# Kernel optimization log

Hardware: AMD Instinct MI355X
Metric: run time of the kernel (lower is better)

## Reference

```python
import jax, jax.numpy as jnp
import numpy as np

B, S, D = 4, 2048, 1024
H = 16
DK = D // H  # 64

def setup_inputs() -> dict:
    key = jax.random.key(0)
    ks = jax.random.split(key, 5)
    scale = 0.02
    return {
        "x": jax.random.normal(ks[0], (B, S, D), dtype=jnp.float32),
        "Wq": jax.random.normal(ks[1], (D, D), dtype=jnp.float32) * scale,
        "Wk": jax.random.normal(ks[2], (D, D), dtype=jnp.float32) * scale,
        "Wv": jax.random.normal(ks[3], (D, D), dtype=jnp.float32) * scale,
        "Wo": jax.random.normal(ks[4], (D, D), dtype=jnp.float32) * scale,
    }

def reference(x, Wq, Wk, Wv, Wo):
    b, s, d = x.shape
    h, dk = H, DK
    # torch nn.Linear(bias=False): y = x @ W.T
    q = (x @ Wq.T).reshape(b, s, h, dk).transpose(0, 2, 1, 3)  # [b,h,s,dk]
    k = (x @ Wk.T).reshape(b, s, h, dk).transpose(0, 2, 1, 3)
    v = (x @ Wv.T).reshape(b, s, h, dk).transpose(0, 2, 1, 3)
    scores = jnp.einsum('bhqd,bhkd->bhqk', q, k) * (dk ** -0.5)
    causal = jnp.triu(jnp.ones((s, s), dtype=bool), k=1)  # True = masked out
    scores = jnp.where(causal, -jnp.inf, scores)
    probs = jax.nn.softmax(scores, axis=-1)
    attn = jnp.einsum('bhqk,bhkd->bhqd', probs, v)  # [b,h,s,dk]
    attn = attn.transpose(0, 2, 1, 3).reshape(b, s, d)
    return attn @ Wo.T
```

## Files before the change

kernel.cpp:

```cpp
#include <hip/hip_runtime.h>

typedef __attribute__((ext_vector_type(8))) short bf16x8;
typedef __attribute__((ext_vector_type(4))) float f32x4;
typedef unsigned int u32;
typedef unsigned short u16;

constexpr int Bb = 4, S = 2048, D = 1024, H = 16, DK = 64, M = Bb * S;

__device__ __forceinline__ u16 f2bf(float f) {
  u32 u = __float_as_uint(f);
  return (u16)((u + 0x7fffu + ((u >> 16) & 1u)) >> 16);
}

__device__ __forceinline__ void gld_lds16(const u16* g, u16* l) {
  __builtin_amdgcn_global_load_lds((const __attribute__((address_space(1))) u32*)g,
                                   (__attribute__((address_space(3))) u32*)l, 16, 0, 0);
}

__global__ void cast_kernel(const float* __restrict__ s, u16* __restrict__ d, int n) {
  int i = (blockIdx.x * blockDim.x + threadIdx.x) * 4;
  if (i >= n) return;
  float4 f = *(const float4*)(s + i);
  ushort4 o;
  o.x = f2bf(f.x); o.y = f2bf(f.y); o.z = f2bf(f.z); o.w = f2bf(f.w);
  *(ushort4*)(d + i) = o;
}

struct CastArgs { const float* s[4]; u16* d[4]; };
__global__ void cast4_kernel(CastArgs a) {
  int i = (blockIdx.x * blockDim.x + threadIdx.x) * 4;
  int w = i >> 20;
  int off = i & ((1 << 20) - 1);
  float4 f = *(const float4*)(a.s[w] + off);
  ushort4 o;
  o.x = f2bf(f.x); o.y = f2bf(f.y); o.z = f2bf(f.z); o.w = f2bf(f.w);
  *(ushort4*)(a.d[w] + off) = o;
}

template <bool OUTF32>
__device__ __forceinline__ void gemm_core(const u16* __restrict__ A,
                                          const u16* __restrict__ Bt,
                                          float* __restrict__ Cf, u16* __restrict__ Cb,
                                          int Nn, int Kk, int m0, int n0,
                                          u16* As, u16* Bs) {
  const int tid = threadIdx.x, wave = tid >> 6, lane = tid & 63;
  const int quad = lane >> 4, col = lane & 15;
  const int wm = wave >> 1, wn = wave & 1;

  f32x4 acc[4][4];
#pragma unroll
  for (int i = 0; i < 4; i++)
#pragma unroll
    for (int j = 0; j < 4; j++) acc[i][j] = (f32x4){0.f, 0.f, 0.f, 0.f};

  for (int k0 = 0; k0 < Kk; k0 += 32) {
#pragma unroll
    for (int j = 0; j < 2; j++) {
      int cb = j * 256 + wave * 64;
      int c = cb + lane;
      const u16* ga = A + (size_t)(m0 + (c >> 2)) * Kk + k0 + (c & 3) * 8;
      gld_lds16(ga, &As[cb * 8]);
      const u16* gb = Bt + (size_t)(n0 + (c >> 2)) * Kk + k0 + (c & 3) * 8;
      gld_lds16(gb, &Bs[cb * 8]);
    }
    __syncthreads();
    bf16x8 af[4], bfr[4];
#pragma unroll
    for (int mi = 0; mi < 4; mi++)
      af[mi] = *(const bf16x8*)&As[(wm * 64 + mi * 16 + col) * 32 + quad * 8];
#pragma unroll
    for (int ni = 0; ni < 4; ni++)
      bfr[ni] = *(const bf16x8*)&Bs[(wn * 64 + ni * 16 + col) * 32 + quad * 8];
#pragma unroll
    for (int mi = 0; mi < 4; mi++)
#pragma unroll
      for (int ni = 0; ni < 4; ni++)
        acc[mi][ni] = __builtin_amdgcn_mfma_f32_16x16x32_bf16(af[mi], bfr[ni], acc[mi][ni], 0, 0, 0);
    __syncthreads();
  }
#pragma unroll
  for (int mi = 0; mi < 4; mi++)
#pragma unroll
    for (int ni = 0; ni < 4; ni++)
#pragma unroll
      for (int r = 0; r < 4; r++) {
        int row = m0 + wm * 64 + mi * 16 + quad * 4 + r;
        int cc = n0 + wn * 64 + ni * 16 + col;
        float v = acc[mi][ni][r];
        if (OUTF32) Cf[(size_t)row * Nn + cc] = v;
        else Cb[(size_t)row * Nn + cc] = f2bf(v);
      }
}

struct QkvArgs { const u16* bt[3]; u16* c[3]; };
__global__ __launch_bounds__(256) void gemm_qkv(const u16* __restrict__ A, QkvArgs q) {
  __shared__ __align__(16) u16 As[128 * 32];
  __shared__ __align__(16) u16 Bs[128 * 32];
  int sel = blockIdx.x >> 3;
  int n0 = (blockIdx.x & 7) * 128, m0 = blockIdx.y * 128;
  gemm_core<false>(A, q.bt[sel], nullptr, q.c[sel], D, D, m0, n0, As, Bs);
}

__global__ __launch_bounds__(256) void gemm_f32(const u16* __restrict__ A,
                                                const u16* __restrict__ Bt,
                                                float* __restrict__ C) {
  __shared__ __align__(16) u16 As[128 * 32];
  __shared__ __align__(16) u16 Bs[128 * 32];
  gemm_core<true>(A, Bt, C, nullptr, D, D, blockIdx.y * 128, blockIdx.x * 128, As, Bs);
}

__global__ __launch_bounds__(256) void attn_kernel(const u16* __restrict__ Q,
                                                   const u16* __restrict__ K,
                                                   const u16* __restrict__ V,
                                                   u16* __restrict__ O) {
  __shared__ __align__(16) u16 Ks[2][2][64 * 32];
  __shared__ __align__(16) u16 Vt[2][64 * 64];
  __shared__ __align__(16) u16 Pw[4][32 * 64];
  const int tid = threadIdx.x, wave = tid >> 6, lane = tid & 63;
  const int quad = lane >> 4, col = lane & 15;
  const int bh = blockIdx.x, b = bh >> 4, h = bh & 15;
  const int qb = (S / 128 - 1) - blockIdx.y;
  const size_t base = (size_t)b * S * D + h * DK;
  const int qw = qb * 128 + wave * 32;

  bf16x8 aq[2][2];
#pragma unroll
  for (int mi = 0; mi < 2; mi++)
#pragma unroll
    for (int kb = 0; kb < 2; kb++)
      aq[mi][kb] = *(const bf16x8*)(Q + base + (size_t)(qw + mi * 16 + col) * D + kb * 32 + quad * 8);

  f32x4 ao[2][4];
#pragma unroll
  for (int mi = 0; mi < 2; mi++)
#pragma unroll
    for (int dg = 0; dg < 4; dg++) ao[mi][dg] = (f32x4){0.f, 0.f, 0.f, 0.f};
  float lp[2][4];
#pragma unroll
  for (int mi = 0; mi < 2; mi++)
#pragma unroll
    for (int r = 0; r < 4; r++) lp[mi][r] = 0.f;

  const int vkey = tid >> 2;
  const int vdof = (tid & 3) * 16;
  const int nkt = 2 * qb + 2;

  bf16x8 vr0, vr1;
  {
    const u16* vp = V + base + (size_t)vkey * D + vdof;
    vr0 = *(const bf16x8*)vp;
    vr1 = *(const bf16x8*)(vp + 8);
  }
  {
    int c = tid, cb = wave * 64;
    const u16* g0 = K + base + (size_t)(c >> 2) * D + (c & 3) * 8;
    gld_lds16(g0, &Ks[0][0][cb * 8]);
    gld_lds16(g0 + 32, &Ks[0][1][cb * 8]);
  }
#pragma unroll
  for (int g = 0; g < 2; g++) {
    int dof = vdof + g * 8;
    int sw = (((vkey >> 3) ^ (dof >> 3)) & 7) * 8 + (vkey & 7);
    bf16x8 vv = g ? vr1 : vr0;
#pragma unroll
    for (int e = 0; e < 8; e++) Vt[0][(dof + e) * 64 + sw] = (u16)vv[e];
  }
  if (nkt > 1) {
    const u16* vp = V + base + (size_t)(64 + vkey) * D + vdof;
    vr0 = *(const bf16x8*)vp;
    vr1 = *(const bf16x8*)(vp + 8);
  }

  for (int kt = 0; kt < nkt; kt++) {
    const int bf = kt & 1;
    __syncthreads();
    if (kt + 1 < nkt) {
      {
        int c = tid, cb = wave * 64;
        const u16* g0 = K + base + (size_t)((kt + 1) * 64 + (c >> 2)) * D + (c & 3) * 8;
        gld_lds16(g0, &Ks[bf ^ 1][0][cb * 8]);
        gld_lds16(g0 + 32, &Ks[bf ^ 1][1][cb * 8]);
      }
#pragma unroll
      for (int g = 0; g < 2; g++) {
        int dof = vdof + g * 8;
        int sw = (((vkey >> 3) ^ (dof >> 3)) & 7) * 8 + (vkey & 7);
        bf16x8 vv = g ? vr1 : vr0;
#pragma unroll
        for (int e = 0; e < 8; e++) Vt[bf ^ 1][(dof + e) * 64 + sw] = (u16)vv[e];
      }
      if (kt + 2 < nkt) {
        const u16* vp = V + base + (size_t)((kt + 2) * 64 + vkey) * D + vdof;
        vr0 = *(const bf16x8*)vp;
        vr1 = *(const bf16x8*)(vp + 8);
      }
    }
    if (kt * 64 <= qw + 31) {
      f32x4 sacc[2][4];
#pragma unroll
      for (int mi = 0; mi < 2; mi++)
#pragma unroll
        for (int n16 = 0; n16 < 4; n16++) sacc[mi][n16] = (f32x4){0.f, 0.f, 0.f, 0.f};
      bf16x8 bk0[4], bk1[4];
#pragma unroll
      for (int n16 = 0; n16 < 4; n16++) {
        bk0[n16] = *(const bf16x8*)&Ks[bf][0][(n16 * 16 + col) * 32 + quad * 8];
        bk1[n16] = *(const bf16x8*)&Ks[bf][1][(n16 * 16 + col) * 32 + quad * 8];
      }
#pragma unroll
      for (int mi = 0; mi < 2; mi++)
#pragma unroll
        for (int n16 = 0; n16 < 4; n16++) {
          sacc[mi][n16] = __builtin_amdgcn_mfma_f32_16x16x32_bf16(aq[mi][0], bk0[n16], sacc[mi][n16], 0, 0, 0);
          sacc[mi][n16] = __builtin_amdgcn_mfma_f32_16x16x32_bf16(aq[mi][1], bk1[n16], sacc[mi][n16], 0, 0, 0);
        }
      const bool needmask = (kt * 64 + 63) > qw;
#pragma unroll
      for (int mi = 0; mi < 2; mi++)
#pragma unroll
        for (int r = 0; r < 4; r++) {
          int qloc = mi * 16 + quad * 4 + r;
          int qs = quad << 1;
#pragma unroll
          for (int n16 = 0; n16 < 4; n16++) {
            int kgl = n16 * 16 + col;
            float p = __expf(sacc[mi][n16][r] * 0.125f);
            if (needmask && (kt * 64 + kgl) > (qw + quad * 4 + r + mi * 16)) p = 0.f;
            lp[mi][r] += p;
            int perm = ((kgl >> 3) ^ qs) & 7;
            Pw[wave][qloc * 64 + perm * 8 + (kgl & 7)] = f2bf(p);
          }
        }
      bf16x8 bv[2][4];
#pragma unroll
      for (int kb = 0; kb < 2; kb++)
#pragma unroll
        for (int dg = 0; dg < 4; dg++) {
          int d3 = (dg * 2 + (col >> 3)) & 7;
          bv[kb][dg] = *(const bf16x8*)&Vt[bf][(dg * 16 + col) * 64 + (((kb * 4 + quad) ^ d3) << 3)];
        }
#pragma unroll
      for (int mi = 0; mi < 2; mi++) {
        int qs = ((col >> 2) & 3) << 1;
        bf16x8 ap0 = *(const bf16x8*)&Pw[wave][(mi * 16 + col) * 64 + (((quad ^ qs) & 7) << 3)];
        bf16x8 ap1 = *(const bf16x8*)&Pw[wave][(mi * 16 + col) * 64 + ((((4 + quad) ^ qs) & 7) << 3)];
#pragma unroll
        for (int dg = 0; dg < 4; dg++) {
          ao[mi][dg] = __builtin_amdgcn_mfma_f32_16x16x32_bf16(ap0, bv[0][dg], ao[mi][dg], 0, 0, 0);
          ao[mi][dg] = __builtin_amdgcn_mfma_f32_16x16x32_bf16(ap1, bv[1][dg], ao[mi][dg], 0, 0, 0);
        }
      }
    }
  }
#pragma unroll
  for (int mi = 0; mi < 2; mi++)
#pragma unroll
    for (int r = 0; r < 4; r++) {
      float l = lp[mi][r];
      l += __shfl_xor(l, 1);
      l += __shfl_xor(l, 2);
      l += __shfl_xor(l, 4);
      l += __shfl_xor(l, 8);
      float inv = 1.f / l;
      int q = qw + mi * 16 + quad * 4 + r;
#pragma unroll
      for (int dg = 0; dg < 4; dg++)
        O[base + (size_t)q * D + dg * 16 + col] = f2bf(ao[mi][dg][r] * inv);
    }
}

extern "C" void kernel_launch(void* const* d_in, const int* in_sizes, int n_in,
                              void* d_out, int out_size, void* d_ws, size_t ws_size,
                              hipStream_t stream) {
  const float* x  = (const float*)d_in[0];
  const float* Wq = (const float*)d_in[1];
  const float* Wk = (const float*)d_in[2];
  const float* Wv = (const float*)d_in[3];
  const float* Wo = (const float*)d_in[4];

  u16* xb  = (u16*)d_ws;
  u16* wqb = xb + (size_t)M * D;
  u16* wkb = wqb + (size_t)D * D;
  u16* wvb = wkb + (size_t)D * D;
  u16* wob = wvb + (size_t)D * D;
  u16* Qb  = wob + (size_t)D * D;
  u16* Kb  = Qb + (size_t)M * D;
  u16* Vb  = Kb + (size_t)M * D;
  u16* Ab  = xb;

  cast_kernel<<<M * D / 1024, 256, 0, stream>>>(x, xb, M * D);
  CastArgs ca;
  ca.s[0] = Wq; ca.s[1] = Wk; ca.s[2] = Wv; ca.s[3] = Wo;
  ca.d[0] = wqb; ca.d[1] = wkb; ca.d[2] = wvb; ca.d[3] = wob;
  cast4_kernel<<<4 * D * D / 1024, 256, 0, stream>>>(ca);

  QkvArgs qa;
  qa.bt[0] = wqb; qa.bt[1] = wkb; qa.bt[2] = wvb;
  qa.c[0] = Qb; qa.c[1] = Kb; qa.c[2] = Vb;
  gemm_qkv<<<dim3(24, M / 128), 256, 0, stream>>>(xb, qa);

  attn_kernel<<<dim3(Bb * H, S / 128), 256, 0, stream>>>(Qb, Kb, Vb, Ab);

  gemm_f32<<<dim3(D / 128, M / 128), 256, 0, stream>>>(Ab, wob, (float*)d_out);
}
```

Baseline: 280.1 us.

## Fold softmax scale into Wq, use exp2, MFMA row sums, swizzled BK64 GEMM

Several independent changes land together. The softmax scale and log2(e) are folded into the Wq cast so attention can use a raw exp2. Row sums are computed with an MFMA against a ones vector, replacing shuffle reductions, and P is truncated to bf16 instead of rounded. K fragments are read straight from global memory instead of being staged in LDS, the K loop is unrolled by two with register double-buffered V, and the causal q-block order is interleaved to balance load. The GEMMs move to BK=64 with XOR-swizzled LDS, doubling LDS use; truncating P and dropping K reuse through LDS may cost accuracy or bandwidth.

New measurement: 298.3 us. 6.5% more time.

```diff
diff --git a/kernel.cpp b/kernel.cpp
--- a/kernel.cpp
+++ b/kernel.cpp
@@ -6,6 +6,12 @@
 typedef unsigned short u16;
 
 constexpr int Bb = 4, S = 2048, D = 1024, H = 16, DK = 64, M = Bb * S;
+
+#if __has_builtin(__builtin_amdgcn_exp2f)
+#define EXP2F __builtin_amdgcn_exp2f
+#else
+#define EXP2F exp2f
+#endif
 
 __device__ __forceinline__ u16 f2bf(float f) {
   u32 u = __float_as_uint(f);
@@ -26,14 +32,15 @@
   *(ushort4*)(d + i) = o;
 }
 
-struct CastArgs { const float* s[4]; u16* d[4]; };
+struct CastArgs { const float* s[4]; u16* d[4]; float sc[4]; };
 __global__ void cast4_kernel(CastArgs a) {
   int i = (blockIdx.x * blockDim.x + threadIdx.x) * 4;
   int w = i >> 20;
   int off = i & ((1 << 20) - 1);
+  float sc = a.sc[w];
   float4 f = *(const float4*)(a.s[w] + off);
   ushort4 o;
-  o.x = f2bf(f.x); o.y = f2bf(f.y); o.z = f2bf(f.z); o.w = f2bf(f.w);
+  o.x = f2bf(f.x * sc); o.y = f2bf(f.y * sc); o.z = f2bf(f.z * sc); o.w = f2bf(f.w * sc);
   *(ushort4*)(a.d[w] + off) = o;
 }
 
@@ -53,29 +60,38 @@
 #pragma unroll
     for (int j = 0; j < 4; j++) acc[i][j] = (f32x4){0.f, 0.f, 0.f, 0.f};
 
-  for (int k0 = 0; k0 < Kk; k0 += 32) {
-#pragma unroll
-    for (int j = 0; j < 2; j++) {
-      int cb = j * 256 + wave * 64;
-      int c = cb + lane;
-      const u16* ga = A + (size_t)(m0 + (c >> 2)) * Kk + k0 + (c & 3) * 8;
-      gld_lds16(ga, &As[cb * 8]);
-      const u16* gb = Bt + (size_t)(n0 + (c >> 2)) * Kk + k0 + (c & 3) * 8;
-      gld_lds16(gb, &Bs[cb * 8]);
+  for (int k0 = 0; k0 < Kk; k0 += 64) {
+#pragma unroll
+    for (int j = 0; j < 4; j++) {
+      int g = (wave * 4 + j) * 64;
+      int gl = g + lane;
+      int r = gl >> 3, sl = gl & 7;
+      int kof = (sl ^ (r & 7)) * 8;
+      const u16* ga = A + (size_t)(m0 + r) * Kk + k0 + kof;
+      gld_lds16(ga, &As[g * 8]);
+      const u16* gb = Bt + (size_t)(n0 + r) * Kk + k0 + kof;
+      gld_lds16(gb, &Bs[g * 8]);
     }
     __syncthreads();
-    bf16x8 af[4], bfr[4];
-#pragma unroll
-    for (int mi = 0; mi < 4; mi++)
-      af[mi] = *(const bf16x8*)&As[(wm * 64 + mi * 16 + col) * 32 + quad * 8];
-#pragma unroll
-    for (int ni = 0; ni < 4; ni++)
-      bfr[ni] = *(const bf16x8*)&Bs[(wn * 64 + ni * 16 + col) * 32 + quad * 8];
-#pragma unroll
-    for (int mi = 0; mi < 4; mi++)
-#pragma unroll
-      for (int ni = 0; ni < 4; ni++)
-        acc[mi][ni] = __builtin_amdgcn_mfma_f32_16x16x32_bf16(af[mi], bfr[ni], acc[mi][ni], 0, 0, 0);
+#pragma unroll
+    for (int kb = 0; kb < 2; kb++) {
+      bf16x8 af[4], bfr[4];
+#pragma unroll
+      for (int mi = 0; mi < 4; mi++) {
+        int R = wm * 64 + mi * 16 + col;
+        af[mi] = *(const bf16x8*)&As[R * 64 + (((kb * 4 + quad) ^ (R & 7)) << 3)];
+      }
+#pragma unroll
+      for (int ni = 0; ni < 4; ni++) {
+        int R = wn * 64 + ni * 16 + col;
+        bfr[ni] = *(const bf16x8*)&Bs[R * 64 + (((kb * 4 + quad) ^ (R & 7)) << 3)];
+      }
+#pragma unroll
+      for (int mi = 0; mi < 4; mi++)
+#pragma unroll
+        for (int ni = 0; ni < 4; ni++)
+          acc[mi][ni] = __builtin_amdgcn_mfma_f32_16x16x32_bf16(af[mi], bfr[ni], acc[mi][ni], 0, 0, 0);
+    }
     __syncthreads();
   }
 #pragma unroll
@@ -94,8 +110,8 @@
 
 struct QkvArgs { const u16* bt[3]; u16* c[3]; };
 __global__ __launch_bounds__(256) void gemm_qkv(const u16* __restrict__ A, QkvArgs q) {
-  __shared__ __align__(16) u16 As[128 * 32];
-  __shared__ __align__(16) u16 Bs[128 * 32];
+  __shared__ __align__(16) u16 As[128 * 64];
+  __shared__ __align__(16) u16 Bs[128 * 64];
   int sel = blockIdx.x >> 3;
   int n0 = (blockIdx.x & 7) * 128, m0 = blockIdx.y * 128;
   gemm_core<false>(A, q.bt[sel], nullptr, q.c[sel], D, D, m0, n0, As, Bs);
@@ -104,8 +120,8 @@
 __global__ __launch_bounds__(256) void gemm_f32(const u16* __restrict__ A,
                                                 const u16* __restrict__ Bt,
                                                 float* __restrict__ C) {
-  __shared__ __align__(16) u16 As[128 * 32];
-  __shared__ __align__(16) u16 Bs[128 * 32];
+  __shared__ __align__(16) u16 As[128 * 64];
+  __shared__ __align__(16) u16 Bs[128 * 64];
   gemm_core<true>(A, Bt, C, nullptr, D, D, blockIdx.y * 128, blockIdx.x * 128, As, Bs);
 }
 
@@ -113,13 +129,13 @@
                                                    const u16* __restrict__ K,
                                                    const u16* __restrict__ V,
                                                    u16* __restrict__ O) {
-  __shared__ __align__(16) u16 Ks[2][2][64 * 32];
   __shared__ __align__(16) u16 Vt[2][64 * 64];
   __shared__ __align__(16) u16 Pw[4][32 * 64];
   const int tid = threadIdx.x, wave = tid >> 6, lane = tid & 63;
   const int quad = lane >> 4, col = lane & 15;
   const int bh = blockIdx.x, b = bh >> 4, h = bh & 15;
-  const int qb = (S / 128 - 1) - blockIdx.y;
+  const int ya = blockIdx.y & 3, yk = blockIdx.y >> 2;
+  const int qb = (yk == 0) ? ya : (yk == 1) ? 7 - ya : (yk == 2) ? 8 + ya : 15 - ya;
   const size_t base = (size_t)b * S * D + h * DK;
   const int qw = qb * 128 + wave * 32;
 
@@ -130,138 +146,129 @@
     for (int kb = 0; kb < 2; kb++)
       aq[mi][kb] = *(const bf16x8*)(Q + base + (size_t)(qw + mi * 16 + col) * D + kb * 32 + quad * 8);
 
-  f32x4 ao[2][4];
-#pragma unroll
-  for (int mi = 0; mi < 2; mi++)
+  f32x4 ao[2][4], lacc[2];
+#pragma unroll
+  for (int mi = 0; mi < 2; mi++) {
+    lacc[mi] = (f32x4){0.f, 0.f, 0.f, 0.f};
 #pragma unroll
     for (int dg = 0; dg < 4; dg++) ao[mi][dg] = (f32x4){0.f, 0.f, 0.f, 0.f};
-  float lp[2][4];
-#pragma unroll
-  for (int mi = 0; mi < 2; mi++)
-#pragma unroll
-    for (int r = 0; r < 4; r++) lp[mi][r] = 0.f;
+  }
+  bf16x8 bones;
+#pragma unroll
+  for (int e = 0; e < 8; e++) bones[e] = (short)0x3F80;
 
   const int vkey = tid >> 2;
   const int vdof = (tid & 3) * 16;
   const int nkt = 2 * qb + 2;
 
-  bf16x8 vr0, vr1;
+  bf16x8 vA0, vA1, vB0, vB1;
   {
     const u16* vp = V + base + (size_t)vkey * D + vdof;
-    vr0 = *(const bf16x8*)vp;
-    vr1 = *(const bf16x8*)(vp + 8);
+    vA0 = *(const bf16x8*)vp; vA1 = *(const bf16x8*)(vp + 8);
   }
   {
-    int c = tid, cb = wave * 64;
-    const u16* g0 = K + base + (size_t)(c >> 2) * D + (c & 3) * 8;
-    gld_lds16(g0, &Ks[0][0][cb * 8]);
-    gld_lds16(g0 + 32, &Ks[0][1][cb * 8]);
-  }
-#pragma unroll
-  for (int g = 0; g < 2; g++) {
-    int dof = vdof + g * 8;
-    int sw = (((vkey >> 3) ^ (dof >> 3)) & 7) * 8 + (vkey & 7);
-    bf16x8 vv = g ? vr1 : vr0;
-#pragma unroll
-    for (int e = 0; e < 8; e++) Vt[0][(dof + e) * 64 + sw] = (u16)vv[e];
-  }
-  if (nkt > 1) {
     const u16* vp = V + base + (size_t)(64 + vkey) * D + vdof;
-    vr0 = *(const bf16x8*)vp;
-    vr1 = *(const bf16x8*)(vp + 8);
-  }
-
-  for (int kt = 0; kt < nkt; kt++) {
-    const int bf = kt & 1;
+    vB0 = *(const bf16x8*)vp; vB1 = *(const bf16x8*)(vp + 8);
+  }
+
+  auto vstage = [&](int buf, bf16x8 v0, bf16x8 v1) {
+#pragma unroll
+    for (int g = 0; g < 2; g++) {
+      int dof = vdof + g * 8;
+      int sw = (((vkey >> 3) ^ (dof >> 3)) & 7) * 8 + (vkey & 7);
+      bf16x8 vv = g ? v1 : v0;
+#pragma unroll
+      for (int e = 0; e < 8; e++) Vt[buf][(dof + e) * 64 + sw] = (u16)vv[e];
+    }
+  };
+  vstage(0, vA0, vA1);
+
+  auto body = [&](int kt, bool ph) {
     __syncthreads();
+    const int bf = ph ? 1 : 0, nb = bf ^ 1;
+    const bool active = (kt * 64 <= qw + 31);
+    bf16x8 bk0[4], bk1[4];
+    if (active) {
+#pragma unroll
+      for (int n16 = 0; n16 < 4; n16++) {
+        const u16* kp = K + base + (size_t)(kt * 64 + n16 * 16 + col) * D + quad * 8;
+        bk0[n16] = *(const bf16x8*)kp;
+        bk1[n16] = *(const bf16x8*)(kp + 32);
+      }
+    }
     if (kt + 1 < nkt) {
-      {
-        int c = tid, cb = wave * 64;
-        const u16* g0 = K + base + (size_t)((kt + 1) * 64 + (c >> 2)) * D + (c & 3) * 8;
-        gld_lds16(g0, &Ks[bf ^ 1][0][cb * 8]);
-        gld_lds16(g0 + 32, &Ks[bf ^ 1][1][cb * 8]);
-      }
-#pragma unroll
-      for (int g = 0; g < 2; g++) {
-        int dof = vdof + g * 8;
-        int sw = (((vkey >> 3) ^ (dof >> 3)) & 7) * 8 + (vkey & 7);
-        bf16x8 vv = g ? vr1 : vr0;
-#pragma unroll
-        for (int e = 0; e < 8; e++) Vt[bf ^ 1][(dof + e) * 64 + sw] = (u16)vv[e];
-      }
+      vstage(nb, ph ? vA0 : vB0, ph ? vA1 : vB1);
       if (kt + 2 < nkt) {
         const u16* vp = V + base + (size_t)((kt + 2) * 64 + vkey) * D + vdof;
-        vr0 = *(const bf16x8*)vp;
-        vr1 = *(const bf16x8*)(vp + 8);
-      }
-    }
-    if (kt * 64 <= qw + 31) {
-      f32x4 sacc[2][4];
-#pragma unroll
-      for (int mi = 0; mi < 2; mi++)
-#pragma unroll
-        for (int n16 = 0; n16 < 4; n16++) sacc[mi][n16] = (f32x4){0.f, 0.f, 0.f, 0.f};
-      bf16x8 bk0[4], bk1[4];
+        if (ph) { vB0 = *(const bf16x8*)vp; vB1 = *(const bf16x8*)(vp + 8); }
+        else    { vA0 = *(const bf16x8*)vp; vA1 = *(const bf16x8*)(vp + 8); }
+      }
+    }
+    if (!active) return;
+    f32x4 sacc[2][4];
+#pragma unroll
+    for (int mi = 0; mi < 2; mi++)
+#pragma unroll
+      for (int n16 = 0; n16 < 4; n16++) sacc[mi][n16] = (f32x4){0.f, 0.f, 0.f, 0.f};
+#pragma unroll
+    for (int mi = 0; mi < 2; mi++)
 #pragma unroll
       for (int n16 = 0; n16 < 4; n16++) {
-        bk0[n16] = *(const bf16x8*)&Ks[bf][0][(n16 * 16 + col) * 32 + quad * 8];
-        bk1[n16] = *(const bf16x8*)&Ks[bf][1][(n16 * 16 + col) * 32 + quad * 8];
-      }
-#pragma unroll
-      for (int mi = 0; mi < 2; mi++)
+        sacc[mi][n16] = __builtin_amdgcn_mfma_f32_16x16x32_bf16(aq[mi][0], bk0[n16], sacc[mi][n16], 0, 0, 0);
+        sacc[mi][n16] = __builtin_amdgcn_mfma_f32_16x16x32_bf16(aq[mi][1], bk1[n16], sacc[mi][n16], 0, 0, 0);
+      }
+    const bool full = (kt * 64 + 63) <= qw;
+#pragma unroll
+    for (int mi = 0; mi < 2; mi++)
+#pragma unroll
+      for (int r = 0; r < 4; r++) {
+        int qloc = mi * 16 + quad * 4 + r;
+        int qs = quad << 1;
 #pragma unroll
         for (int n16 = 0; n16 < 4; n16++) {
-          sacc[mi][n16] = __builtin_amdgcn_mfma_f32_16x16x32_bf16(aq[mi][0], bk0[n16], sacc[mi][n16], 0, 0, 0);
-          sacc[mi][n16] = __builtin_amdgcn_mfma_f32_16x16x32_bf16(aq[mi][1], bk1[n16], sacc[mi][n16], 0, 0, 0);
+          float p = EXP2F(sacc[mi][n16][r]);
+          if (!full) {
+            int kg = kt * 64 + n16 * 16 + col;
+            p = (kg > qw + qloc) ? 0.f : p;
+          }
+          int kgl = n16 * 16 + col;
+          int perm = ((kgl >> 3) ^ qs) & 7;
+          Pw[wave][qloc * 64 + perm * 8 + (kgl & 7)] = (u16)(__float_as_uint(p) >> 16);
         }
-      const bool needmask = (kt * 64 + 63) > qw;
-#pragma unroll
-      for (int mi = 0; mi < 2; mi++)
-#pragma unroll
-        for (int r = 0; r < 4; r++) {
-          int qloc = mi * 16 + quad * 4 + r;
-          int qs = quad << 1;
-#pragma unroll
-          for (int n16 = 0; n16 < 4; n16++) {
-            int kgl = n16 * 16 + col;
-            float p = __expf(sacc[mi][n16][r] * 0.125f);
-            if (needmask && (kt * 64 + kgl) > (qw + quad * 4 + r + mi * 16)) p = 0.f;
-            lp[mi][r] += p;
-            int perm = ((kgl >> 3) ^ qs) & 7;
-            Pw[wave][qloc * 64 + perm * 8 + (kgl & 7)] = f2bf(p);
-          }
-        }
-      bf16x8 bv[2][4];
-#pragma unroll
-      for (int kb = 0; kb < 2; kb++)
-#pragma unroll
-        for (int dg = 0; dg < 4; dg++) {
-          int d3 = (dg * 2 + (col >> 3)) & 7;
-          bv[kb][dg] = *(const bf16x8*)&Vt[bf][(dg * 16 + col) * 64 + (((kb * 4 + quad) ^ d3) << 3)];
-        }
-#pragma unroll
-      for (int mi = 0; mi < 2; mi++) {
-        int qs = ((col >> 2) & 3) << 1;
-        bf16x8 ap0 = *(const bf16x8*)&Pw[wave][(mi * 16 + col) * 64 + (((quad ^ qs) & 7) << 3)];
-        bf16x8 ap1 = *(const bf16x8*)&Pw[wave][(mi * 16 + col) * 64 + ((((4 + quad) ^ qs) & 7) << 3)];
-#pragma unroll
-        for (int dg = 0; dg < 4; dg++) {
-          ao[mi][dg] = __builtin_amdgcn_mfma_f32_16x16x32_bf16(ap0, bv[0][dg], ao[mi][dg], 0, 0, 0);
-          ao[mi][dg] = __builtin_amdgcn_mfma_f32_16x16x32_bf16(ap1, bv[1][dg], ao[mi][dg], 0, 0, 0);
-        }
-      }
-    }
-  }
+      }
+    bf16x8 bv[2][4];
+#pragma unroll
+    for (int kb = 0; kb < 2; kb++)
+#pragma unroll
+      for (int dg = 0; dg < 4; dg++) {
+        int d3 = (dg * 2 + (col >> 3)) & 7;
+        bv[kb][dg] = *(const bf16x8*)&Vt[bf][(dg * 16 + col) * 64 + (((kb * 4 + quad) ^ d3) << 3)];
+      }
+#pragma unroll
+    for (int mi = 0; mi < 2; mi++) {
+      int qs2 = ((col >> 2) & 3) << 1;
+      bf16x8 ap0 = *(const bf16x8*)&Pw[wave][(mi * 16 + col) * 64 + (((quad ^ qs2) & 7) << 3)];
+      bf16x8 ap1 = *(const bf16x8*)&Pw[wave][(mi * 16 + col) * 64 + ((((4 + quad) ^ qs2) & 7) << 3)];
+#pragma unroll
+      for (int dg = 0; dg < 4; dg++) {
+        ao[mi][dg] = __builtin_amdgcn_mfma_f32_16x16x32_bf16(ap0, bv[0][dg], ao[mi][dg], 0, 0, 0);
+        ao[mi][dg] = __builtin_amdgcn_mfma_f32_16x16x32_bf16(ap1, bv[1][dg], ao[mi][dg], 0, 0, 0);
+      }
+      lacc[mi] = __builtin_amdgcn_mfma_f32_16x16x32_bf16(ap0, bones, lacc[mi], 0, 0, 0);
+      lacc[mi] = __builtin_amdgcn_mfma_f32_16x16x32_bf16(ap1, bones, lacc[mi], 0, 0, 0);
+    }
+  };
+
+  for (int kt = 0; kt < nkt; kt += 2) {
+    body(kt, false);
+    body(kt + 1, true);
+  }
+
 #pragma unroll
   for (int mi = 0; mi < 2; mi++)
 #pragma unroll
     for (int r = 0; r < 4; r++) {
-      float l = lp[mi][r];
-      l += __shfl_xor(l, 1);
-      l += __shfl_xor(l, 2);
-      l += __shfl_xor(l, 4);
-      l += __shfl_xor(l, 8);
-      float inv = 1.f / l;
+      float inv = 1.f / lacc[mi][r];
       int q = qw + mi * 16 + quad * 4 + r;
 #pragma unroll
       for (int dg = 0; dg < 4; dg++)
@@ -292,6 +299,8 @@
   CastArgs ca;
   ca.s[0] = Wq; ca.s[1] = Wk; ca.s[2] = Wv; ca.s[3] = Wo;
   ca.d[0] = wqb; ca.d[1] = wkb; ca.d[2] = wvb; ca.d[3] = wob;
+  ca.sc[0] = 0.18033688011112042f;
+  ca.sc[1] = 1.f; ca.sc[2] = 1.f; ca.sc[3] = 1.f;
   cast4_kernel<<<4 * D * D / 1024, 256, 0, stream>>>(ca);
 
   QkvArgs qa;
```
